# Kernel tuning notes

Measured on AMD Instinct MI355X. Metric: run time of the kernel, lower is better.

Reference implementation:

```python
import jax, jax.numpy as jnp
import numpy as np

N_TOKENS = 32768
DIM = 2048
N_EXPERTS = 64
TOP_K = 8
N_GROUP = 8
TOPK_GROUP = 4
ROUTE_SCALE = 2.5
EPS = 1e-20


def setup_inputs() -> dict:
    key = jax.random.key(0)
    k1, k2 = jax.random.split(key)
    hidden_states = jax.random.normal(k1, (N_TOKENS, DIM), dtype=jnp.float32)
    weight = jax.random.normal(k2, (N_EXPERTS, DIM), dtype=jnp.float32) * 0.02
    e_score_correction_bias = jnp.zeros((N_EXPERTS,), dtype=jnp.float32)
    return {"hidden_states": hidden_states, "weight": weight,
            "e_score_correction_bias": e_score_correction_bias}


def reference(hidden_states, weight, e_score_correction_bias):
    # router logits in fp32: [N, E]
    logits = jnp.einsum('nd,ed->ne', hidden_states.astype(jnp.float32),
                        weight.astype(jnp.float32))
    scores = jax.nn.sigmoid(logits)  # score_func == 'sigmoid'

    # --- top-k index selection (no-grad path in torch) ---
    sfc = scores + e_score_correction_bias[None, :]  # [N, E]
    per_group = N_EXPERTS // N_GROUP
    # group score = sum of top-2 scores within each group: [N, G]
    grouped = sfc.reshape(-1, N_GROUP, per_group)
    group_scores = jax.lax.top_k(grouped, 2)[0].sum(axis=-1)
    # pick top `TOPK_GROUP` groups
    _, group_idx = jax.lax.top_k(group_scores, TOPK_GROUP)  # [N, topk_group]
    n = group_scores.shape[0]
    group_mask = jnp.zeros_like(group_scores).at[
        jnp.arange(n)[:, None], group_idx].set(1.0)  # [N, G]
    score_mask = jnp.repeat(group_mask, per_group, axis=1)  # [N, E]
    masked_scores = jnp.where(score_mask > 0, sfc, 0.0)
    _, topk_indices = jax.lax.top_k(masked_scores, TOP_K)  # [N, top_k]

    # gather weights from *unbiased* scores, normalize, scale
    topk_weights = jnp.take_along_axis(scores, topk_indices, axis=1)
    denom = topk_weights.sum(axis=-1, keepdims=True) + EPS
    topk_weights = topk_weights / denom * ROUTE_SCALE
    return topk_indices, topk_weights
```

## Files before the change

### kernel.cpp

```cpp
#include <hip/hip_runtime.h>
#include <math.h>

#define NT 32768
#define DIM 2048
#define NE 64
#define RSCALE 2.5f
#define REPS 1e-20f
#define KC 32
#define NCH (DIM / KC)
#define TOK 64

#define HL_BUF 12288
#define WL_OFF 24576
#define BS_OFF 49152
#define ARENA 49408

typedef __attribute__((ext_vector_type(8))) short short8x;
typedef __attribute__((ext_vector_type(4))) float f32x4;
typedef __attribute__((ext_vector_type(4))) unsigned int uint4x;

#define PACKHI(odd, even) __builtin_amdgcn_perm((odd), (even), 0x07060302u)

__device__ __forceinline__ void decomp4(f32x4 x, unsigned int o[6]) {
    unsigned int u0 = __float_as_uint(x.x), u1 = __float_as_uint(x.y);
    unsigned int u2 = __float_as_uint(x.z), u3 = __float_as_uint(x.w);
    o[0] = PACKHI(u1, u0); o[1] = PACKHI(u3, u2);
    float r0 = x.x - __uint_as_float(u0 & 0xffff0000u);
    float r1 = x.y - __uint_as_float(u1 & 0xffff0000u);
    float r2 = x.z - __uint_as_float(u2 & 0xffff0000u);
    float r3 = x.w - __uint_as_float(u3 & 0xffff0000u);
    unsigned int v0 = __float_as_uint(r0), v1 = __float_as_uint(r1);
    unsigned int v2 = __float_as_uint(r2), v3 = __float_as_uint(r3);
    o[2] = PACKHI(v1, v0); o[3] = PACKHI(v3, v2);
    float s0 = r0 - __uint_as_float(v0 & 0xffff0000u);
    float s1 = r1 - __uint_as_float(v1 & 0xffff0000u);
    float s2 = r2 - __uint_as_float(v2 & 0xffff0000u);
    float s3 = r3 - __uint_as_float(v3 & 0xffff0000u);
    o[4] = PACKHI(__float_as_uint(s1), __float_as_uint(s0));
    o[5] = PACKHI(__float_as_uint(s3), __float_as_uint(s2));
}

__device__ __forceinline__ void decomp8(f32x4 a, f32x4 b,
                                        short8x* f0, short8x* f1, short8x* f2) {
    unsigned int oa[6], ob[6];
    decomp4(a, oa); decomp4(b, ob);
    uint4x t0 = {oa[0], oa[1], ob[0], ob[1]};
    uint4x t1 = {oa[2], oa[3], ob[2], ob[3]};
    uint4x t2 = {oa[4], oa[5], ob[4], ob[5]};
    *f0 = __builtin_bit_cast(short8x, t0);
    *f1 = __builtin_bit_cast(short8x, t1);
    *f2 = __builtin_bit_cast(short8x, t2);
}

#define BARRIER() do { \
    asm volatile("s_waitcnt lgkmcnt(0)" ::: "memory"); \
    __builtin_amdgcn_s_barrier(); \
    __builtin_amdgcn_sched_barrier(0); \
} while (0)

#define STAGE_ISSUE(SA, SB, KOFF) do { \
    SA = *(const f32x4*)(gsrc + (KOFF));     \
    SB = *(const f32x4*)(gsrc + (KOFF) + 4); \
} while (0)

#define STAGE_WRITE(SA, SB, PN) do { \
    short8x f0_, f1_, f2_; \
    decomp8(SA, SB, &f0_, &f1_, &f2_); \
    *(short8x*)(arena + sbase + (PN) * HL_BUF + 0 * 4096 + soff) = f0_; \
    *(short8x*)(arena + sbase + (PN) * HL_BUF + 1 * 4096 + soff) = f1_; \
    *(short8x*)(arena + sbase + (PN) * HL_BUF + 2 * 4096 + soff) = f2_; \
} while (0)

#define COMPUTE(P) do { \
    const char* hb = arena + (P) * HL_BUF; \
    const char* wb = arena + WL_OFF + (P) * HL_BUF; \
    short8x a0, a1, a2; \
    { const int t_ = tt * 16 + l15; \
      const int ro_ = t_ * 64 + ((g ^ ((t_ >> 1) & 3)) << 4); \
      a0 = *(const short8x*)(hb + 0 * 4096 + ro_); \
      a1 = *(const short8x*)(hb + 1 * 4096 + ro_); \
      a2 = *(const short8x*)(hb + 2 * 4096 + ro_); } \
    _Pragma("unroll") \
    for (int et = 0; et < 2; ++et) { \
        const int e_ = ep * 32 + et * 16 + l15; \
        const int ro_ = e_ * 64 + ((g ^ ((e_ >> 1) & 3)) << 4); \
        short8x b0 = *(const short8x*)(wb + 0 * 4096 + ro_); \
        short8x b1 = *(const short8x*)(wb + 1 * 4096 + ro_); \
        short8x b2 = *(const short8x*)(wb + 2 * 4096 + ro_); \
        Cm[et] = __builtin_amdgcn_mfma_f32_16x16x32_bf16(a0, b0, Cm[et], 0, 0, 0); \
        Cc[et] = __builtin_amdgcn_mfma_f32_16x16x32_bf16(a1, b0, Cc[et], 0, 0, 0); \
        Cc[et] = __builtin_amdgcn_mfma_f32_16x16x32_bf16(a2, b0, Cc[et], 0, 0, 0); \
        Cc[et] = __builtin_amdgcn_mfma_f32_16x16x32_bf16(a0, b1, Cc[et], 0, 0, 0); \
        Cc[et] = __builtin_amdgcn_mfma_f32_16x16x32_bf16(a1, b1, Cc[et], 0, 0, 0); \
        Cc[et] = __builtin_amdgcn_mfma_f32_16x16x32_bf16(a0, b2, Cc[et], 0, 0, 0); \
    } \
} while (0)

#define DRAIN do { \
    _Pragma("unroll") \
    for (int et = 0; et < 2; ++et) { \
        _Pragma("unroll") \
        for (int r = 0; r < 4; ++r) \
            md[et][r] += (double)Cm[et][r] + (double)Cc[et][r]; \
        Cm[et] = (f32x4)0.0f; Cc[et] = (f32x4)0.0f; \
    } \
} while (0)

__global__ __launch_bounds__(512, 4) void router_kernel(
    const float* __restrict__ H,
    const float* __restrict__ W,
    const float* __restrict__ B,
    float* __restrict__ out)
{
    __shared__ __align__(16) char arena[ARENA];
    float* bsf = (float*)(arena + BS_OFF);
    float* scf = (float*)(arena);

    const int tid  = threadIdx.x;
    const int lane = tid & 63;
    const int w    = __builtin_amdgcn_readfirstlane(tid >> 6);
    const int l15  = lane & 15, g = lane >> 4;
    const size_t tb = (size_t)blockIdx.x * TOK;

    if (tid < NE) bsf[tid] = B[tid];

    const int si   = tid & 255;
    const int srow = si >> 2;
    const int sq   = si & 3;
    const bool isH = tid < 256;
    const float* gsrc = isH ? (H + (tb + (size_t)srow) * DIM + sq * 8)
                            : (W + (size_t)srow * DIM + sq * 8);
    const int sbase = isH ? 0 : WL_OFF;
    const int soff  = srow * 64 + ((sq ^ ((srow >> 1) & 3)) << 4);

    const int tt = w & 3, ep = w >> 2;

    f32x4 Cm[2], Cc[2];
    double md[2][4];
    #pragma unroll
    for (int et = 0; et < 2; ++et) {
        Cm[et] = (f32x4)0.0f; Cc[et] = (f32x4)0.0f;
        #pragma unroll
        for (int r = 0; r < 4; ++r) md[et][r] = 0.0;
    }

    f32x4 sA0, sA1, sB0, sB1;

    STAGE_ISSUE(sA0, sA1, 0);
    STAGE_WRITE(sA0, sA1, 0);
    STAGE_ISSUE(sB0, sB1, KC);
    BARRIER();

    for (int chb = 0; chb < NCH; chb += 2) {
        if (chb + 2 < NCH) STAGE_ISSUE(sA0, sA1, (chb + 2) * KC);
        COMPUTE(0);
        STAGE_WRITE(sB0, sB1, 1);
        BARRIER();

        if (chb + 3 < NCH) STAGE_ISSUE(sB0, sB1, (chb + 3) * KC);
        COMPUTE(1);
        if (chb + 2 < NCH) STAGE_WRITE(sA0, sA1, 0);
        if (((chb + 1) & 7) == 7) DRAIN;
        BARRIER();
    }

    #pragma unroll
    for (int et = 0; et < 2; ++et)
        #pragma unroll
        for (int r = 0; r < 4; ++r) {
            float logit = (float)md[et][r];
            float s = 1.0f / (1.0f + expf(-logit));
            int t = tt * 16 + g * 4 + r;
            int e = ep * 32 + et * 16 + l15;
            scf[t * 65 + e] = s;
        }
    __syncthreads();

    if ((tid & 7) == 0) {
        const int t = tid >> 3;
        const float* sc = &scf[t * 65];
        float gs[8];
        #pragma unroll
        for (int gg = 0; gg < 8; ++gg) {
            float m1 = -1e30f, m2 = -1e30f;
            #pragma unroll
            for (int j = 0; j < 8; ++j) {
                float v = sc[gg * 8 + j] + bsf[gg * 8 + j];
                if (v > m1) { m2 = m1; m1 = v; }
                else if (v > m2) { m2 = v; }
            }
            gs[gg] = m1 + m2;
        }
        unsigned gmask = 0;
        for (int i = 0; i < 4; ++i) {
            float best = -1e30f; int bg = 0;
            for (int gg = 0; gg < 8; ++gg)
                if (!((gmask >> gg) & 1u) && gs[gg] > best) { best = gs[gg]; bg = gg; }
            gmask |= 1u << bg;
        }
        unsigned long long picked = 0ull;
        int   idxs[8];
        float wts[8];
        float wsum = 0.0f;
        for (int i = 0; i < 8; ++i) {
            float best = -1e30f; int bi = 0;
            for (int e = 0; e < 64; ++e) {
                if ((picked >> e) & 1ull) continue;
                float v = ((gmask >> (e >> 3)) & 1u) ? (sc[e] + bsf[e]) : 0.0f;
                if (v > best) { best = v; bi = e; }
            }
            picked |= 1ull << bi;
            idxs[i] = bi;
            wts[i] = sc[bi];
            wsum += sc[bi];
        }
        const float scale = RSCALE / (wsum + REPS);
        const size_t token = tb + t;
        #pragma unroll
        for (int i = 0; i < 8; ++i) {
            out[token * 8 + i] = (float)idxs[i];
            out[(size_t)NT * 8 + token * 8 + i] = wts[i] * scale;
        }
    }
}

extern "C" void kernel_launch(void* const* d_in, const int* in_sizes, int n_in,
                              void* d_out, int out_size, void* d_ws, size_t ws_size,
                              hipStream_t stream) {
    (void)in_sizes; (void)n_in; (void)out_size; (void)d_ws; (void)ws_size;
    const float* H = (const float*)d_in[0];
    const float* W = (const float*)d_in[1];
    const float* B = (const float*)d_in[2];
    float* out = (float*)d_out;
    router_kernel<<<dim3(NT / TOK), dim3(512), 0, stream>>>(H, W, B, out);
}
```

Baseline: 140.4 us.

## Halve block to 256 threads with 2x2 register tiles per wave

Shrinks each block from 8 to 4 waves. Every wave now computes a 32x32 tile (two token sub-tiles by two expert sub-tiles), so each A and B fragment loaded from LDS feeds twice as many MFMAs. Each thread stages both an H row slice and a W row slice per chunk. This is meant to cut LDS read traffic per MFMA and barrier overhead, at the cost of more accumulator registers (including doubles) and fewer waves per block, which may reduce latency hiding.

```diff
diff --git a/kernel.cpp b/kernel.cpp
--- a/kernel.cpp
+++ b/kernel.cpp
@@ -58,55 +58,69 @@
     __builtin_amdgcn_sched_barrier(0); \
 } while (0)
 
-#define STAGE_ISSUE(SA, SB, KOFF) do { \
-    SA = *(const f32x4*)(gsrc + (KOFF));     \
-    SB = *(const f32x4*)(gsrc + (KOFF) + 4); \
-} while (0)
-
-#define STAGE_WRITE(SA, SB, PN) do { \
+#define STAGE_ISSUE(HA, HB, WA, WB, KOFF) do { \
+    HA = *(const f32x4*)(hgsrc + (KOFF));     \
+    HB = *(const f32x4*)(hgsrc + (KOFF) + 4); \
+    WA = *(const f32x4*)(wgsrc + (KOFF));     \
+    WB = *(const f32x4*)(wgsrc + (KOFF) + 4); \
+} while (0)
+
+#define STAGE_WRITE(HA, HB, WA, WB, PN) do { \
     short8x f0_, f1_, f2_; \
-    decomp8(SA, SB, &f0_, &f1_, &f2_); \
-    *(short8x*)(arena + sbase + (PN) * HL_BUF + 0 * 4096 + soff) = f0_; \
-    *(short8x*)(arena + sbase + (PN) * HL_BUF + 1 * 4096 + soff) = f1_; \
-    *(short8x*)(arena + sbase + (PN) * HL_BUF + 2 * 4096 + soff) = f2_; \
+    decomp8(HA, HB, &f0_, &f1_, &f2_); \
+    *(short8x*)(arena + (PN) * HL_BUF + 0 * 4096 + soff) = f0_; \
+    *(short8x*)(arena + (PN) * HL_BUF + 1 * 4096 + soff) = f1_; \
+    *(short8x*)(arena + (PN) * HL_BUF + 2 * 4096 + soff) = f2_; \
+    decomp8(WA, WB, &f0_, &f1_, &f2_); \
+    *(short8x*)(arena + WL_OFF + (PN) * HL_BUF + 0 * 4096 + soff) = f0_; \
+    *(short8x*)(arena + WL_OFF + (PN) * HL_BUF + 1 * 4096 + soff) = f1_; \
+    *(short8x*)(arena + WL_OFF + (PN) * HL_BUF + 2 * 4096 + soff) = f2_; \
 } while (0)
 
 #define COMPUTE(P) do { \
     const char* hb = arena + (P) * HL_BUF; \
     const char* wb = arena + WL_OFF + (P) * HL_BUF; \
-    short8x a0, a1, a2; \
-    { const int t_ = tt * 16 + l15; \
-      const int ro_ = t_ * 64 + ((g ^ ((t_ >> 1) & 3)) << 4); \
-      a0 = *(const short8x*)(hb + 0 * 4096 + ro_); \
-      a1 = *(const short8x*)(hb + 1 * 4096 + ro_); \
-      a2 = *(const short8x*)(hb + 2 * 4096 + ro_); } \
+    short8x a0[2], a1[2], a2[2]; \
+    _Pragma("unroll") \
+    for (int tt = 0; tt < 2; ++tt) { \
+        const int t_ = wr * 32 + tt * 16 + l15; \
+        const int ro_ = t_ * 64 + ((g ^ ((t_ >> 1) & 3)) << 4); \
+        a0[tt] = *(const short8x*)(hb + 0 * 4096 + ro_); \
+        a1[tt] = *(const short8x*)(hb + 1 * 4096 + ro_); \
+        a2[tt] = *(const short8x*)(hb + 2 * 4096 + ro_); \
+    } \
     _Pragma("unroll") \
     for (int et = 0; et < 2; ++et) { \
-        const int e_ = ep * 32 + et * 16 + l15; \
+        const int e_ = wc * 32 + et * 16 + l15; \
         const int ro_ = e_ * 64 + ((g ^ ((e_ >> 1) & 3)) << 4); \
         short8x b0 = *(const short8x*)(wb + 0 * 4096 + ro_); \
         short8x b1 = *(const short8x*)(wb + 1 * 4096 + ro_); \
         short8x b2 = *(const short8x*)(wb + 2 * 4096 + ro_); \
-        Cm[et] = __builtin_amdgcn_mfma_f32_16x16x32_bf16(a0, b0, Cm[et], 0, 0, 0); \
-        Cc[et] = __builtin_amdgcn_mfma_f32_16x16x32_bf16(a1, b0, Cc[et], 0, 0, 0); \
-        Cc[et] = __builtin_amdgcn_mfma_f32_16x16x32_bf16(a2, b0, Cc[et], 0, 0, 0); \
-        Cc[et] = __builtin_amdgcn_mfma_f32_16x16x32_bf16(a0, b1, Cc[et], 0, 0, 0); \
-        Cc[et] = __builtin_amdgcn_mfma_f32_16x16x32_bf16(a1, b1, Cc[et], 0, 0, 0); \
-        Cc[et] = __builtin_amdgcn_mfma_f32_16x16x32_bf16(a0, b2, Cc[et], 0, 0, 0); \
+        _Pragma("unroll") \
+        for (int tt = 0; tt < 2; ++tt) { \
+            Cm[tt][et] = __builtin_amdgcn_mfma_f32_16x16x32_bf16(a0[tt], b0, Cm[tt][et], 0, 0, 0); \
+            Cc[tt][et] = __builtin_amdgcn_mfma_f32_16x16x32_bf16(a1[tt], b0, Cc[tt][et], 0, 0, 0); \
+            Cc[tt][et] = __builtin_amdgcn_mfma_f32_16x16x32_bf16(a2[tt], b0, Cc[tt][et], 0, 0, 0); \
+            Cc[tt][et] = __builtin_amdgcn_mfma_f32_16x16x32_bf16(a0[tt], b1, Cc[tt][et], 0, 0, 0); \
+            Cc[tt][et] = __builtin_amdgcn_mfma_f32_16x16x32_bf16(a1[tt], b1, Cc[tt][et], 0, 0, 0); \
+            Cc[tt][et] = __builtin_amdgcn_mfma_f32_16x16x32_bf16(a0[tt], b2, Cc[tt][et], 0, 0, 0); \
+        } \
     } \
 } while (0)
 
 #define DRAIN do { \
     _Pragma("unroll") \
-    for (int et = 0; et < 2; ++et) { \
+    for (int tt = 0; tt < 2; ++tt) \
         _Pragma("unroll") \
-        for (int r = 0; r < 4; ++r) \
-            md[et][r] += (double)Cm[et][r] + (double)Cc[et][r]; \
-        Cm[et] = (f32x4)0.0f; Cc[et] = (f32x4)0.0f; \
-    } \
-} while (0)
-
-__global__ __launch_bounds__(512, 4) void router_kernel(
+        for (int et = 0; et < 2; ++et) { \
+            _Pragma("unroll") \
+            for (int r = 0; r < 4; ++r) \
+                md[tt][et][r] += (double)Cm[tt][et][r] + (double)Cc[tt][et][r]; \
+            Cm[tt][et] = (f32x4)0.0f; Cc[tt][et] = (f32x4)0.0f; \
+        } \
+} while (0)
+
+__global__ __launch_bounds__(256, 2) void router_kernel(
     const float* __restrict__ H,
     const float* __restrict__ W,
     const float* __restrict__ B,
@@ -124,60 +138,61 @@
 
     if (tid < NE) bsf[tid] = B[tid];
 
-    const int si   = tid & 255;
-    const int srow = si >> 2;
-    const int sq   = si & 3;
-    const bool isH = tid < 256;
-    const float* gsrc = isH ? (H + (tb + (size_t)srow) * DIM + sq * 8)
-                            : (W + (size_t)srow * DIM + sq * 8);
-    const int sbase = isH ? 0 : WL_OFF;
-    const int soff  = srow * 64 + ((sq ^ ((srow >> 1) & 3)) << 4);
-
-    const int tt = w & 3, ep = w >> 2;
-
-    f32x4 Cm[2], Cc[2];
-    double md[2][4];
+    const int srow = tid >> 2;
+    const int sq   = tid & 3;
+    const float* hgsrc = H + (tb + (size_t)srow) * DIM + sq * 8;
+    const float* wgsrc = W + (size_t)srow * DIM + sq * 8;
+    const int soff = srow * 64 + ((sq ^ ((srow >> 1) & 3)) << 4);
+
+    const int wr = w & 1, wc = w >> 1;
+
+    f32x4 Cm[2][2], Cc[2][2];
+    double md[2][2][4];
     #pragma unroll
-    for (int et = 0; et < 2; ++et) {
-        Cm[et] = (f32x4)0.0f; Cc[et] = (f32x4)0.0f;
-        #pragma unroll
-        for (int r = 0; r < 4; ++r) md[et][r] = 0.0;
-    }
-
-    f32x4 sA0, sA1, sB0, sB1;
-
-    STAGE_ISSUE(sA0, sA1, 0);
-    STAGE_WRITE(sA0, sA1, 0);
-    STAGE_ISSUE(sB0, sB1, KC);
+    for (int tt = 0; tt < 2; ++tt)
+        #pragma unroll
+        for (int et = 0; et < 2; ++et) {
+            Cm[tt][et] = (f32x4)0.0f; Cc[tt][et] = (f32x4)0.0f;
+            #pragma unroll
+            for (int r = 0; r < 4; ++r) md[tt][et][r] = 0.0;
+        }
+
+    f32x4 hA0, hA1, wA0, wA1, hB0, hB1, wB0, wB1;
+
+    STAGE_ISSUE(hA0, hA1, wA0, wA1, 0);
+    STAGE_WRITE(hA0, hA1, wA0, wA1, 0);
+    STAGE_ISSUE(hB0, hB1, wB0, wB1, KC);
     BARRIER();
 
     for (int chb = 0; chb < NCH; chb += 2) {
-        if (chb + 2 < NCH) STAGE_ISSUE(sA0, sA1, (chb + 2) * KC);
+        if (chb + 2 < NCH) STAGE_ISSUE(hA0, hA1, wA0, wA1, (chb + 2) * KC);
         COMPUTE(0);
-        STAGE_WRITE(sB0, sB1, 1);
+        STAGE_WRITE(hB0, hB1, wB0, wB1, 1);
         BARRIER();
 
-        if (chb + 3 < NCH) STAGE_ISSUE(sB0, sB1, (chb + 3) * KC);
+        if (chb + 3 < NCH) STAGE_ISSUE(hB0, hB1, wB0, wB1, (chb + 3) * KC);
         COMPUTE(1);
-        if (chb + 2 < NCH) STAGE_WRITE(sA0, sA1, 0);
+        if (chb + 2 < NCH) STAGE_WRITE(hA0, hA1, wA0, wA1, 0);
         if (((chb + 1) & 7) == 7) DRAIN;
         BARRIER();
     }
 
     #pragma unroll
-    for (int et = 0; et < 2; ++et)
-        #pragma unroll
-        for (int r = 0; r < 4; ++r) {
-            float logit = (float)md[et][r];
-            float s = 1.0f / (1.0f + expf(-logit));
-            int t = tt * 16 + g * 4 + r;
-            int e = ep * 32 + et * 16 + l15;
-            scf[t * 65 + e] = s;
-        }
+    for (int tt = 0; tt < 2; ++tt)
+        #pragma unroll
+        for (int et = 0; et < 2; ++et)
+            #pragma unroll
+            for (int r = 0; r < 4; ++r) {
+                float logit = (float)md[tt][et][r];
+                float s = 1.0f / (1.0f + expf(-logit));
+                int t = wr * 32 + tt * 16 + g * 4 + r;
+                int e = wc * 32 + et * 16 + l15;
+                scf[t * 65 + e] = s;
+            }
     __syncthreads();
 
-    if ((tid & 7) == 0) {
-        const int t = tid >> 3;
+    if ((tid & 3) == 0) {
+        const int t = tid >> 2;
         const float* sc = &scf[t * 65];
         float gs[8];
         #pragma unroll
@@ -232,5 +247,5 @@
     const float* W = (const float*)d_in[1];
     const float* B = (const float*)d_in[2];
     float* out = (float*)d_out;
-    router_kernel<<<dim3(NT / TOK), dim3(512), 0, stream>>>(H, W, B, out);
-}
+    router_kernel<<<dim3(NT / TOK), dim3(256), 0, stream>>>(H, W, B, out);
+}
```

Measured after the change: 131.7 us. 6.2% less time.

## Retile router GEMM to 32-token blocks with 64-wide K chunks

Applied to the files above, without the earlier changes.

Each block now handles 32 tokens with 256 threads instead of 64 tokens with 512. Each wave owns 16 experts across both 16-token tiles, and K chunks grow from 32 to 64 with a new XOR swizzle. The double-buffered LDS staging becomes a single buffer guarded by extra barriers. This shrinks LDS per block so more blocks fit per CU, but every block reloads the full weight matrix, which doubles weight traffic, and the added barriers reduce load/compute overlap.

```diff
diff --git a/kernel.cpp b/kernel.cpp
--- a/kernel.cpp
+++ b/kernel.cpp
@@ -6,14 +6,13 @@
 #define NE 64
 #define RSCALE 2.5f
 #define REPS 1e-20f
-#define KC 32
-#define NCH (DIM / KC)
-#define TOK 64
-
-#define HL_BUF 12288
-#define WL_OFF 24576
-#define BS_OFF 49152
-#define ARENA 49408
+#define KC 64
+#define NCHK (DIM / KC)
+#define TOKB 32
+
+#define WL_OFF 12288
+#define BS_OFF 36864
+#define ARENA 37120
 
 typedef __attribute__((ext_vector_type(8))) short short8x;
 typedef __attribute__((ext_vector_type(4))) float f32x4;
@@ -58,55 +57,71 @@
     __builtin_amdgcn_sched_barrier(0); \
 } while (0)
 
-#define STAGE_ISSUE(SA, SB, KOFF) do { \
-    SA = *(const f32x4*)(gsrc + (KOFF));     \
-    SB = *(const f32x4*)(gsrc + (KOFF) + 4); \
-} while (0)
-
-#define STAGE_WRITE(SA, SB, PN) do { \
+#define STAGE_ISSUE(H0, H1, W0, W1, W2, W3, KOFF) do { \
+    H0 = *(const f32x4*)(hgsrc + (KOFF)); \
+    H1 = *(const f32x4*)(hgsrc + (KOFF) + 4); \
+    W0 = *(const f32x4*)(wgsrc + (KOFF)); \
+    W1 = *(const f32x4*)(wgsrc + (KOFF) + 4); \
+    W2 = *(const f32x4*)(wgsrc + (KOFF) + 8); \
+    W3 = *(const f32x4*)(wgsrc + (KOFF) + 12); \
+} while (0)
+
+#define STAGE_WRITE(H0, H1, W0, W1, W2, W3) do { \
     short8x f0_, f1_, f2_; \
-    decomp8(SA, SB, &f0_, &f1_, &f2_); \
-    *(short8x*)(arena + sbase + (PN) * HL_BUF + 0 * 4096 + soff) = f0_; \
-    *(short8x*)(arena + sbase + (PN) * HL_BUF + 1 * 4096 + soff) = f1_; \
-    *(short8x*)(arena + sbase + (PN) * HL_BUF + 2 * 4096 + soff) = f2_; \
-} while (0)
-
-#define COMPUTE(P) do { \
-    const char* hb = arena + (P) * HL_BUF; \
-    const char* wb = arena + WL_OFF + (P) * HL_BUF; \
-    short8x a0, a1, a2; \
-    { const int t_ = tt * 16 + l15; \
-      const int ro_ = t_ * 64 + ((g ^ ((t_ >> 1) & 3)) << 4); \
-      a0 = *(const short8x*)(hb + 0 * 4096 + ro_); \
-      a1 = *(const short8x*)(hb + 1 * 4096 + ro_); \
-      a2 = *(const short8x*)(hb + 2 * 4096 + ro_); } \
+    decomp8(H0, H1, &f0_, &f1_, &f2_); \
+    *(short8x*)(arena + 0    + hoff) = f0_; \
+    *(short8x*)(arena + 4096 + hoff) = f1_; \
+    *(short8x*)(arena + 8192 + hoff) = f2_; \
+    decomp8(W0, W1, &f0_, &f1_, &f2_); \
+    *(short8x*)(arena + WL_OFF + 0     + woff0) = f0_; \
+    *(short8x*)(arena + WL_OFF + 8192  + woff0) = f1_; \
+    *(short8x*)(arena + WL_OFF + 16384 + woff0) = f2_; \
+    decomp8(W2, W3, &f0_, &f1_, &f2_); \
+    *(short8x*)(arena + WL_OFF + 0     + woff1) = f0_; \
+    *(short8x*)(arena + WL_OFF + 8192  + woff1) = f1_; \
+    *(short8x*)(arena + WL_OFF + 16384 + woff1) = f2_; \
+} while (0)
+
+#define COMPUTE() do { \
     _Pragma("unroll") \
-    for (int et = 0; et < 2; ++et) { \
-        const int e_ = ep * 32 + et * 16 + l15; \
-        const int ro_ = e_ * 64 + ((g ^ ((e_ >> 1) & 3)) << 4); \
-        short8x b0 = *(const short8x*)(wb + 0 * 4096 + ro_); \
-        short8x b1 = *(const short8x*)(wb + 1 * 4096 + ro_); \
-        short8x b2 = *(const short8x*)(wb + 2 * 4096 + ro_); \
-        Cm[et] = __builtin_amdgcn_mfma_f32_16x16x32_bf16(a0, b0, Cm[et], 0, 0, 0); \
-        Cc[et] = __builtin_amdgcn_mfma_f32_16x16x32_bf16(a1, b0, Cc[et], 0, 0, 0); \
-        Cc[et] = __builtin_amdgcn_mfma_f32_16x16x32_bf16(a2, b0, Cc[et], 0, 0, 0); \
-        Cc[et] = __builtin_amdgcn_mfma_f32_16x16x32_bf16(a0, b1, Cc[et], 0, 0, 0); \
-        Cc[et] = __builtin_amdgcn_mfma_f32_16x16x32_bf16(a1, b1, Cc[et], 0, 0, 0); \
-        Cc[et] = __builtin_amdgcn_mfma_f32_16x16x32_bf16(a0, b2, Cc[et], 0, 0, 0); \
+    for (int kk = 0; kk < 2; ++kk) { \
+        short8x a0[2], a1[2], a2[2]; \
+        _Pragma("unroll") \
+        for (int tt = 0; tt < 2; ++tt) { \
+            const int r_ = tt * 16 + l15; \
+            const int sb = r_ * 128 + (((kk * 4 + g) ^ (r_ & 7)) << 4); \
+            a0[tt] = *(const short8x*)(arena + 0    + sb); \
+            a1[tt] = *(const short8x*)(arena + 4096 + sb); \
+            a2[tt] = *(const short8x*)(arena + 8192 + sb); \
+        } \
+        const int rw = w * 16 + l15; \
+        const int wb = rw * 128 + (((kk * 4 + g) ^ (rw & 7)) << 4); \
+        short8x b0 = *(const short8x*)(arena + WL_OFF + 0     + wb); \
+        short8x b1 = *(const short8x*)(arena + WL_OFF + 8192  + wb); \
+        short8x b2 = *(const short8x*)(arena + WL_OFF + 16384 + wb); \
+        _Pragma("unroll") \
+        for (int tt = 0; tt < 2; ++tt) { \
+            Cm[tt] = __builtin_amdgcn_mfma_f32_16x16x32_bf16(a0[tt], b0, Cm[tt], 0, 0, 0); \
+            Cc[tt] = __builtin_amdgcn_mfma_f32_16x16x32_bf16(a1[tt], b0, Cc[tt], 0, 0, 0); \
+            Cc[tt] = __builtin_amdgcn_mfma_f32_16x16x32_bf16(a2[tt], b0, Cc[tt], 0, 0, 0); \
+            Cc[tt] = __builtin_amdgcn_mfma_f32_16x16x32_bf16(a0[tt], b1, Cc[tt], 0, 0, 0); \
+            Cc[tt] = __builtin_amdgcn_mfma_f32_16x16x32_bf16(a1[tt], b1, Cc[tt], 0, 0, 0); \
+            Cc[tt] = __builtin_amdgcn_mfma_f32_16x16x32_bf16(a0[tt], b2, Cc[tt], 0, 0, 0); \
+        } \
     } \
 } while (0)
 
 #define DRAIN do { \
     _Pragma("unroll") \
-    for (int et = 0; et < 2; ++et) { \
+    for (int tt = 0; tt < 2; ++tt) { \
         _Pragma("unroll") \
         for (int r = 0; r < 4; ++r) \
-            md[et][r] += (double)Cm[et][r] + (double)Cc[et][r]; \
-        Cm[et] = (f32x4)0.0f; Cc[et] = (f32x4)0.0f; \
+            md[tt][r] += (double)Cm[tt][r] + (double)Cc[tt][r]; \
+        Cm[tt] = (f32x4)0.0f; Cc[tt] = (f32x4)0.0f; \
     } \
 } while (0)
 
-__global__ __launch_bounds__(512, 4) void router_kernel(
+__global__ __launch_bounds__(256, 4) void router_kernel(
     const float* __restrict__ H,
     const float* __restrict__ W,
     const float* __restrict__ B,
@@ -120,58 +135,58 @@
     const int lane = tid & 63;
     const int w    = __builtin_amdgcn_readfirstlane(tid >> 6);
     const int l15  = lane & 15, g = lane >> 4;
-    const size_t tb = (size_t)blockIdx.x * TOK;
+    const size_t tb = (size_t)blockIdx.x * TOKB;
 
     if (tid < NE) bsf[tid] = B[tid];
 
-    const int si   = tid & 255;
-    const int srow = si >> 2;
-    const int sq   = si & 3;
-    const bool isH = tid < 256;
-    const float* gsrc = isH ? (H + (tb + (size_t)srow) * DIM + sq * 8)
-                            : (W + (size_t)srow * DIM + sq * 8);
-    const int sbase = isH ? 0 : WL_OFF;
-    const int soff  = srow * 64 + ((sq ^ ((srow >> 1) & 3)) << 4);
-
-    const int tt = w & 3, ep = w >> 2;
+    const int hrow = tid >> 3, hq = tid & 7;
+    const int wrow = tid >> 2, wq = (tid & 3) << 1;
+    const float* hgsrc = H + (tb + (size_t)hrow) * DIM + hq * 8;
+    const float* wgsrc = W + (size_t)wrow * DIM + wq * 8;
+    const int hoff  = hrow * 128 + ((hq ^ (hrow & 7)) << 4);
+    const int woff0 = wrow * 128 + ((wq ^ (wrow & 7)) << 4);
+    const int woff1 = wrow * 128 + (((wq + 1) ^ (wrow & 7)) << 4);
 
     f32x4 Cm[2], Cc[2];
     double md[2][4];
     #pragma unroll
-    for (int et = 0; et < 2; ++et) {
-        Cm[et] = (f32x4)0.0f; Cc[et] = (f32x4)0.0f;
-        #pragma unroll
-        for (int r = 0; r < 4; ++r) md[et][r] = 0.0;
+    for (int tt = 0; tt < 2; ++tt) {
+        Cm[tt] = (f32x4)0.0f; Cc[tt] = (f32x4)0.0f;
+        #pragma unroll
+        for (int r = 0; r < 4; ++r) md[tt][r] = 0.0;
     }
 
-    f32x4 sA0, sA1, sB0, sB1;
-
-    STAGE_ISSUE(sA0, sA1, 0);
-    STAGE_WRITE(sA0, sA1, 0);
-    STAGE_ISSUE(sB0, sB1, KC);
+    f32x4 hA0, hA1, wA0, wA1, wA2, wA3;
+    f32x4 hB0, hB1, wB0, wB1, wB2, wB3;
+
+    STAGE_ISSUE(hA0, hA1, wA0, wA1, wA2, wA3, 0);
+    STAGE_ISSUE(hB0, hB1, wB0, wB1, wB2, wB3, KC);
+    STAGE_WRITE(hA0, hA1, wA0, wA1, wA2, wA3);
     BARRIER();
 
-    for (int chb = 0; chb < NCH; chb += 2) {
-        if (chb + 2 < NCH) STAGE_ISSUE(sA0, sA1, (chb + 2) * KC);
-        COMPUTE(0);
-        STAGE_WRITE(sB0, sB1, 1);
-        BARRIER();
-
-        if (chb + 3 < NCH) STAGE_ISSUE(sB0, sB1, (chb + 3) * KC);
-        COMPUTE(1);
-        if (chb + 2 < NCH) STAGE_WRITE(sA0, sA1, 0);
-        if (((chb + 1) & 7) == 7) DRAIN;
+    for (int chb = 0; chb < NCHK; chb += 2) {
+        COMPUTE();
+        if (chb + 2 < NCHK) STAGE_ISSUE(hA0, hA1, wA0, wA1, wA2, wA3, (chb + 2) * KC);
+        BARRIER();
+        STAGE_WRITE(hB0, hB1, wB0, wB1, wB2, wB3);
+        BARRIER();
+
+        COMPUTE();
+        if (chb + 3 < NCHK) STAGE_ISSUE(hB0, hB1, wB0, wB1, wB2, wB3, (chb + 3) * KC);
+        if (((chb + 1) & 3) == 3) DRAIN;
+        BARRIER();
+        if (chb + 2 < NCHK) STAGE_WRITE(hA0, hA1, wA0, wA1, wA2, wA3);
         BARRIER();
     }
 
     #pragma unroll
-    for (int et = 0; et < 2; ++et)
+    for (int tt = 0; tt < 2; ++tt)
         #pragma unroll
         for (int r = 0; r < 4; ++r) {
-            float logit = (float)md[et][r];
+            float logit = (float)md[tt][r];
             float s = 1.0f / (1.0f + expf(-logit));
             int t = tt * 16 + g * 4 + r;
-            int e = ep * 32 + et * 16 + l15;
+            int e = w * 16 + l15;
             scf[t * 65 + e] = s;
         }
     __syncthreads();
@@ -232,5 +247,5 @@
     const float* W = (const float*)d_in[1];
     const float* B = (const float*)d_in[2];
     float* out = (float*)d_out;
-    router_kernel<<<dim3(NT / TOK), dim3(512), 0, stream>>>(H, W, B, out);
-}
+    router_kernel<<<dim3(NT / TOKB), dim3(256), 0, stream>>>(H, W, B, out);
+}
```

Measured after the change: 148.9 us. 6.0% more time.
